# Kernel optimization log

Hardware: AMD Instinct MI355X
Metric: run time of the kernel (lower is better)

The kernel has to match this reference:

```python
import jax, jax.numpy as jnp
import numpy as np
from jax.scipy.special import logsumexp

B, T, D, H, K = 32, 512, 768, 256, 32


def setup_inputs() -> dict:
    key = jax.random.key(0)
    ks = jax.random.split(key, 12)
    x = jax.random.normal(ks[0], (B, T, D), jnp.float32)
    lengths = jax.random.randint(ks[1], (B,), T // 2, T + 1).astype(jnp.int32)
    mask = jnp.arange(T)[None, :] < lengths[:, None]  # [B,T] bool
    targets = jax.random.randint(ks[2], (B, T), 0, K)

    def p(k, shape, fan):
        return jax.random.normal(k, shape, jnp.float32) / np.sqrt(fan).astype(np.float32)

    W_ih_f = p(ks[3], (4 * H, D), D); W_hh_f = p(ks[4], (4 * H, H), H)
    W_ih_b = p(ks[5], (4 * H, D), D); W_hh_b = p(ks[6], (4 * H, H), H)
    b_f = jnp.zeros((4 * H,), jnp.float32); b_b = jnp.zeros((4 * H,), jnp.float32)
    W_clf = p(ks[7], (K, 2 * H), 2 * H); b_clf = jnp.zeros((K,), jnp.float32)
    start_t = jax.random.uniform(ks[8], (K,), jnp.float32, -0.1, 0.1)
    end_t = jax.random.uniform(ks[9], (K,), jnp.float32, -0.1, 0.1)
    trans = jax.random.uniform(ks[10], (K, K), jnp.float32, -0.1, 0.1)
    return {"input": x, "lengths": lengths, "mask": mask, "targets": targets,
            "W_ih_f": W_ih_f, "W_hh_f": W_hh_f, "b_f": b_f,
            "W_ih_b": W_ih_b, "W_hh_b": W_hh_b, "b_b": b_b,
            "W_clf": W_clf, "b_clf": b_clf,
            "start_t": start_t, "end_t": end_t, "trans": trans}


def _lstm_dir(x_tbd, W_ih, W_hh, b):
    # x_tbd: [T,B,D] -> hs [T,B,H], torch gate order (i,f,g,o)
    Hh = W_hh.shape[1]
    pre = jnp.einsum('tbd,gd->tbg', x_tbd, W_ih) + b  # precompute input projections

    def step(carry, p_t):
        h, c = carry
        g = p_t + h @ W_hh.T
        i, f, gg, o = jnp.split(g, 4, axis=-1)
        c = jax.nn.sigmoid(f) * c + jax.nn.sigmoid(i) * jnp.tanh(gg)
        h = jax.nn.sigmoid(o) * jnp.tanh(c)
        return (h, c), h

    b_sz = x_tbd.shape[1]
    init = (jnp.zeros((b_sz, Hh), x_tbd.dtype), jnp.zeros((b_sz, Hh), x_tbd.dtype))
    _, hs = jax.lax.scan(step, init, pre)
    return hs


def _emissions(x, lengths, W_ih_f, W_hh_f, b_f, W_ih_b, W_hh_b, b_b, W_clf, b_clf):
    Tn = x.shape[1]
    t_idx = jnp.arange(Tn)[None, :]
    # per-sequence reversal of the valid prefix (emulates packed bidirectional LSTM)
    rev_idx = jnp.where(t_idx < lengths[:, None], lengths[:, None] - 1 - t_idx, t_idx)
    h_f = _lstm_dir(x.transpose(1, 0, 2), W_ih_f, W_hh_f, b_f).transpose(1, 0, 2)
    x_rev = jnp.take_along_axis(x, rev_idx[:, :, None], axis=1)
    h_b = _lstm_dir(x_rev.transpose(1, 0, 2), W_ih_b, W_hh_b, b_b).transpose(1, 0, 2)
    h_b = jnp.take_along_axis(h_b, rev_idx[:, :, None], axis=1)  # un-flip
    hcat = jnp.concatenate([h_f, h_b], axis=-1)  # [B,T,2H]
    return hcat @ W_clf.T + b_clf  # [B,T,K]


def _crf_nll(em, targets, mask, lengths, start_t, end_t, trans):
    maskf = mask.astype(em.dtype)
    # numerator (gold path score)
    em_sc = jnp.take_along_axis(em, targets[:, :, None], axis=2)[..., 0]  # [B,T]
    tr_sc = trans[targets[:, :-1], targets[:, 1:]]  # [B,T-1]
    num = start_t[targets[:, 0]] + em_sc[:, 0] + jnp.sum((tr_sc + em_sc[:, 1:]) * maskf[:, 1:], axis=1)
    last_tags = jnp.take_along_axis(targets, (lengths - 1).astype(targets.dtype)[:, None], axis=1)[:, 0]
    num = num + end_t[last_tags]
    # log partition via forward algorithm
    def fwd_step(alpha, inp):
        e_t, m_t = inp
        nxt = logsumexp(alpha[:, :, None] + trans[None] + e_t[:, None, :], axis=1)
        return jnp.where(m_t[:, None], nxt, alpha), None

    alpha0 = start_t[None] + em[:, 0]
    alpha, _ = jax.lax.scan(fwd_step, alpha0, (em[:, 1:].transpose(1, 0, 2), mask[:, 1:].T))
    logZ = logsumexp(alpha + end_t[None], axis=1)
    return -jnp.mean(num - logZ)


def _viterbi(em, mask, start_t, end_t, trans):
    Kn = trans.shape[0]

    def vit_step(score, inp):
        e_t, m_t = inp
        bc = score[:, :, None] + trans[None] + e_t[:, None, :]  # [B,Kprev,Kcur]
        nxt = jnp.max(bc, axis=1)
        idx = jnp.argmax(bc, axis=1)  # [B,K] best previous tag
        idx = jnp.where(m_t[:, None], idx, jnp.arange(Kn)[None, :])  # identity on pads
        return jnp.where(m_t[:, None], nxt, score), idx

    score0 = start_t[None] + em[:, 0]
    score, hist = jax.lax.scan(vit_step, score0, (em[:, 1:].transpose(1, 0, 2), mask[:, 1:].T))
    last = jnp.argmax(score + end_t[None], axis=1)  # [B]

    def back(tag, h):
        prev = jnp.take_along_axis(h, tag[:, None], axis=1)[:, 0]
        return prev, prev

    _, tags_prev = jax.lax.scan(back, last, hist, reverse=True)  # [T-1,B]
    tags = jnp.concatenate([tags_prev, last[None]], axis=0).T  # [B,T]
    return jnp.where(mask, tags, 0)  # zero_pad


def reference(input, lengths, mask, targets, W_ih_f, W_hh_f, b_f, W_ih_b, W_hh_b, b_b,
              W_clf, b_clf, start_t, end_t, trans):
    em = _emissions(input, lengths, W_ih_f, W_hh_f, b_f, W_ih_b, W_hh_b, b_b, W_clf, b_clf)
    loss = _crf_nll(em, targets, mask, lengths, start_t, end_t, trans)
    preds = _viterbi(em, mask, start_t, end_t, trans)
    return loss, preds
```

## Files before the change

kernel.cpp:

```cpp
#include <hip/hip_runtime.h>
#include <hip/hip_bf16.h>


#define NB 32
#define NT 512
#define ND 768
#define NH 256
#define NK 32

__global__ __launch_bounds__(256) void k_sgemm(const float* __restrict__ A,
                                               const float* __restrict__ Wf,
                                               const float* __restrict__ Wb,
                                               float* __restrict__ C) {
    __shared__ float As[2][16][132];
    __shared__ float Bs[2][16][132];
    const int tid = threadIdx.x;
    const int bx = blockIdx.x;
    const int by = blockIdx.y;
    const int tx = tid & 15, ty = tid >> 4;
    const int sm = tid >> 2;
    const int sk = (tid & 3) * 4;
    float acc[8][8];
#pragma unroll
    for (int i = 0; i < 8; ++i)
#pragma unroll
        for (int j = 0; j < 8; ++j) acc[i][j] = 0.f;

    const float* Arow0 = A + (size_t)(by * 128 + sm) * ND + sk;
    const float* Arow1 = A + (size_t)(by * 128 + 64 + sm) * ND + sk;
    const int gn0 = bx * 128 + sm, gn1 = gn0 + 64;
    const float* W0 = (gn0 < 1024) ? (Wf + (size_t)gn0 * ND + sk) : (Wb + (size_t)(gn0 - 1024) * ND + sk);
    const float* W1 = (gn1 < 1024) ? (Wf + (size_t)gn1 * ND + sk) : (Wb + (size_t)(gn1 - 1024) * ND + sk);

    {
        float4 a0 = *(const float4*)(Arow0);
        float4 a1 = *(const float4*)(Arow1);
        float4 w0 = *(const float4*)(W0);
        float4 w1 = *(const float4*)(W1);
        As[0][sk + 0][sm] = a0.x; As[0][sk + 1][sm] = a0.y; As[0][sk + 2][sm] = a0.z; As[0][sk + 3][sm] = a0.w;
        As[0][sk + 0][64 + sm] = a1.x; As[0][sk + 1][64 + sm] = a1.y; As[0][sk + 2][64 + sm] = a1.z; As[0][sk + 3][64 + sm] = a1.w;
        Bs[0][sk + 0][sm] = w0.x; Bs[0][sk + 1][sm] = w0.y; Bs[0][sk + 2][sm] = w0.z; Bs[0][sk + 3][sm] = w0.w;
        Bs[0][sk + 0][64 + sm] = w1.x; Bs[0][sk + 1][64 + sm] = w1.y; Bs[0][sk + 2][64 + sm] = w1.z; Bs[0][sk + 3][64 + sm] = w1.w;
    }
    __syncthreads();

    int cur = 0;
    for (int k0 = 0; k0 < ND; k0 += 16) {
        const bool more = (k0 + 16) < ND;
        float4 na0, na1, nw0, nw1;
        if (more) {
            na0 = *(const float4*)(Arow0 + k0 + 16);
            na1 = *(const float4*)(Arow1 + k0 + 16);
            nw0 = *(const float4*)(W0 + k0 + 16);
            nw1 = *(const float4*)(W1 + k0 + 16);
        }
#pragma unroll
        for (int kk = 0; kk < 16; ++kk) {
            float a[8], b[8];
            *(float4*)&a[0] = *(const float4*)&As[cur][kk][ty * 4];
            *(float4*)&a[4] = *(const float4*)&As[cur][kk][64 + ty * 4];
            *(float4*)&b[0] = *(const float4*)&Bs[cur][kk][tx * 4];
            *(float4*)&b[4] = *(const float4*)&Bs[cur][kk][64 + tx * 4];
#pragma unroll
            for (int i = 0; i < 8; ++i)
#pragma unroll
                for (int j = 0; j < 8; ++j)
                    acc[i][j] = fmaf(a[i], b[j], acc[i][j]);
        }
        if (more) {
            const int nxt = cur ^ 1;
            As[nxt][sk + 0][sm] = na0.x; As[nxt][sk + 1][sm] = na0.y; As[nxt][sk + 2][sm] = na0.z; As[nxt][sk + 3][sm] = na0.w;
            As[nxt][sk + 0][64 + sm] = na1.x; As[nxt][sk + 1][64 + sm] = na1.y; As[nxt][sk + 2][64 + sm] = na1.z; As[nxt][sk + 3][64 + sm] = na1.w;
            Bs[nxt][sk + 0][sm] = nw0.x; Bs[nxt][sk + 1][sm] = nw0.y; Bs[nxt][sk + 2][sm] = nw0.z; Bs[nxt][sk + 3][sm] = nw0.w;
            Bs[nxt][sk + 0][64 + sm] = nw1.x; Bs[nxt][sk + 1][64 + sm] = nw1.y; Bs[nxt][sk + 2][64 + sm] = nw1.z; Bs[nxt][sk + 3][64 + sm] = nw1.w;
            __syncthreads();
            cur = nxt;
        }
    }
#pragma unroll
    for (int i = 0; i < 8; ++i) {
        int m = by * 128 + ((i < 4) ? (ty * 4 + i) : (64 + ty * 4 + (i - 4)));
        float* Crow = C + (size_t)m * 2048 + bx * 128;
        *(float4*)(Crow + tx * 4)      = make_float4(acc[i][0], acc[i][1], acc[i][2], acc[i][3]);
        *(float4*)(Crow + 64 + tx * 4) = make_float4(acc[i][4], acc[i][5], acc[i][6], acc[i][7]);
    }
}

__global__ __launch_bounds__(256) void k_wt4(const float* __restrict__ Whf,
                                             const float* __restrict__ Whb,
                                             float4* __restrict__ Wt4) {
    int gid = blockIdx.x * 256 + threadIdx.x;
    if (gid >= 131072) return;
    int dir = gid >> 16;
    int k   = (gid >> 8) & 255;
    int j   = gid & 255;
    const float* W = dir ? Whb : Whf;
    Wt4[gid] = make_float4(W[(size_t)(0 * 256 + j) * 256 + k],
                           W[(size_t)(1 * 256 + j) * 256 + k],
                           W[(size_t)(2 * 256 + j) * 256 + k],
                           W[(size_t)(3 * 256 + j) * 256 + k]);
}

__device__ __forceinline__ float sigm(float x) { return 1.f / (1.f + expf(-x)); }

__global__ __launch_bounds__(256, 1) void k_lstm6(const float* __restrict__ C,
                                                  const float4* __restrict__ Wt4,
                                                  const float* __restrict__ b_f,
                                                  const float* __restrict__ b_b,
                                                  const int* __restrict__ lengths,
                                                  float* __restrict__ h_f,
                                                  float* __restrict__ h_b) {
    __shared__ float4 wlds[36][256];
    __shared__ float hsh[4][272];
    const int tid = threadIdx.x;
    const int g = blockIdx.x & 63, s = blockIdx.x >> 6;
    const int b = g & 31, dir = g >> 5;
    const int j0 = s * 64;
    const float* bias = dir ? b_b : b_f;
    float* hdir = dir ? h_b : h_f;

    const int j = tid >> 2;
    const int kq = tid & 3;
    const int w = tid >> 6;
    const int lane = tid & 63;

    float4 wreg[28];
    {
        const float4* wb = Wt4 + ((size_t)dir * 256 + kq * 64) * 256 + j0 + j;
#pragma unroll
        for (int u = 0; u < 28; ++u) wreg[u] = wb[(size_t)u * 256];
#pragma unroll
        for (int u = 0; u < 36; ++u) wlds[u][tid] = wb[(size_t)(28 + u) * 256];
    }
    float4 breg = make_float4(0.f, 0.f, 0.f, 0.f);
    if (kq == 0)
        breg = make_float4(bias[j0 + j], bias[256 + j0 + j],
                           bias[512 + j0 + j], bias[768 + j0 + j]);
    const int mylen = lengths[b];
    float creg = 0.f;
    __syncthreads();

    for (int t = 0; t < NT; ++t) {
        float4 pre = make_float4(0.f, 0.f, 0.f, 0.f);
        if (kq == 0) {
            int src_t = t;
            if (dir) src_t = (t < mylen) ? (mylen - 1 - t) : t;
            const float* Crow = C + (size_t)(b * 512 + src_t) * 2048 + dir * 1024 + j0 + j;
            pre.x = Crow[0]; pre.y = Crow[256]; pre.z = Crow[512]; pre.w = Crow[768];
        }
        float4 acc = make_float4(0.f, 0.f, 0.f, 0.f);
        if (t > 0) {
            const float* hp = hdir + ((size_t)b * 512 + (t - 1)) * 256 + 4 * lane;
            unsigned long long u0, u1;
            int guard = 0;
            for (;;) {
                u0 = __hip_atomic_load((const unsigned long long*)hp,
                                       __ATOMIC_RELAXED, __HIP_MEMORY_SCOPE_AGENT);
                u1 = __hip_atomic_load((const unsigned long long*)(hp + 2),
                                       __ATOMIC_RELAXED, __HIP_MEMORY_SCOPE_AGENT);
                if ((unsigned)(u0 & 0xFFFFFFFFu) != 0xFFFFFFFFu &&
                    (unsigned)(u0 >> 32)        != 0xFFFFFFFFu &&
                    (unsigned)(u1 & 0xFFFFFFFFu) != 0xFFFFFFFFu &&
                    (unsigned)(u1 >> 32)        != 0xFFFFFFFFu) break;
                if (++guard > (1 << 22)) break;
            }
            const int d0 = 4 * lane;
            float* dst = &hsh[w][(d0 >> 6) * 68 + (d0 & 63)];
            *(float4*)dst = make_float4(
                __uint_as_float((unsigned)(u0 & 0xFFFFFFFFu)),
                __uint_as_float((unsigned)(u0 >> 32)),
                __uint_as_float((unsigned)(u1 & 0xFFFFFFFFu)),
                __uint_as_float((unsigned)(u1 >> 32)));
            asm volatile("s_waitcnt lgkmcnt(0)" ::: "memory");
            __builtin_amdgcn_sched_barrier(0);
            const float* src = &hsh[w][kq * 68];
#pragma unroll
            for (int c = 0; c < 16; ++c) {
                float ha[4];
                *(float4*)ha = *(const float4*)(src + 4 * c);
#pragma unroll
                for (int i = 0; i < 4; ++i) {
                    float4 wv = (c < 7) ? wreg[c * 4 + i] : wlds[(c - 7) * 4 + i][tid];
                    acc.x = fmaf(wv.x, ha[i], acc.x);
                    acc.y = fmaf(wv.y, ha[i], acc.y);
                    acc.z = fmaf(wv.z, ha[i], acc.z);
                    acc.w = fmaf(wv.w, ha[i], acc.w);
                }
            }
        }
        if (kq == 0) {
            acc.x += pre.x + breg.x; acc.y += pre.y + breg.y;
            acc.z += pre.z + breg.z; acc.w += pre.w + breg.w;
        }
#pragma unroll
        for (int off = 1; off <= 2; off <<= 1) {
            acc.x += __shfl_xor(acc.x, off);
            acc.y += __shfl_xor(acc.y, off);
            acc.z += __shfl_xor(acc.z, off);
            acc.w += __shfl_xor(acc.w, off);
        }
        float ig = sigm(acc.x), fg = sigm(acc.y), gt = tanhf(acc.z), og = sigm(acc.w);
        creg = fg * creg + ig * gt;
        float hn = og * tanhf(creg);
        if (kq == 0)
            __hip_atomic_store(hdir + ((size_t)b * 512 + t) * 256 + j0 + j, hn,
                               __ATOMIC_RELAXED, __HIP_MEMORY_SCOPE_AGENT);
    }
}

__global__ __launch_bounds__(256) void k_em(const float* __restrict__ hf,
                                            const float* __restrict__ hb,
                                            const float* __restrict__ Wclf,
                                            const float* __restrict__ bclf,
                                            const int* __restrict__ lengths,
                                            float* __restrict__ em) {
    extern __shared__ float4 wc4[];
    const int tid = threadIdx.x;
    for (int idx = tid; idx < 4096; idx += 256) {
        int jq = idx >> 5, ko = idx & 31;
        wc4[idx] = *(const float4*)(Wclf + (size_t)ko * 512 + jq * 4);
    }
    __syncthreads();
    const int r = tid >> 5, ko = tid & 31;
    const int m = blockIdx.x * 8 + r;
    const int b = m >> 9, t = m & 511;
    const int len = lengths[b];
    const int rev = (t < len) ? (len - 1 - t) : t;
    const float* hfr = hf + (size_t)m * 256;
    const float* hbr = hb + (size_t)(b * 512 + rev) * 256;
    float acc = bclf[ko];
#pragma unroll 4
    for (int jq = 0; jq < 64; ++jq) {
        float4 h4 = *(const float4*)(hfr + jq * 4);
        float4 ww = wc4[jq * 32 + ko];
        acc += h4.x * ww.x + h4.y * ww.y + h4.z * ww.z + h4.w * ww.w;
    }
#pragma unroll 4
    for (int jq = 0; jq < 64; ++jq) {
        float4 h4 = *(const float4*)(hbr + jq * 4);
        float4 ww = wc4[(64 + jq) * 32 + ko];
        acc += h4.x * ww.x + h4.y * ww.y + h4.z * ww.z + h4.w * ww.w;
    }
    em[(size_t)m * 32 + ko] = acc;
}

__global__ __launch_bounds__(64) void k_crfvit(const float* __restrict__ em,
                                               const int* __restrict__ targets,
                                               const int* __restrict__ lengths,
                                               const float* __restrict__ start_t,
                                               const float* __restrict__ end_t,
                                               const float* __restrict__ trans,
                                               float* __restrict__ numv,
                                               float* __restrict__ logZv,
                                               float* __restrict__ out) {
    __shared__ float trans_s[32][33];
    __shared__ float vec[32];
    __shared__ unsigned char hist[511 * 32];
    const int tid = threadIdx.x;
    const int b = blockIdx.x & 31;
    const int mode = blockIdx.x >> 5;
    for (int idx = tid; idx < 1024; idx += 64) trans_s[idx >> 5][idx & 31] = trans[idx];
    const int len = lengths[b];
    const float* emb = em + (size_t)b * 512 * 32;
    const int k = tid & 31, half = tid >> 5;
    if (tid < 32) vec[tid] = start_t[tid] + emb[tid];

    if (mode == 0) {
        float e_cur = emb[32 + k];
        for (int t = 1; t < NT; ++t) {
            float e_next = (t + 1 < NT) ? emb[(t + 1) * 32 + k] : 0.f;
            bool mv = t < len;
            int kp0 = half * 16;
            float m = -1e30f;
#pragma unroll 4
            for (int i = 0; i < 16; ++i)
                m = fmaxf(m, vec[kp0 + i] + trans_s[kp0 + i][k]);
            float m2 = fmaxf(m, __shfl_xor(m, 32));
            float ssum = 0.f;
#pragma unroll 4
            for (int i = 0; i < 16; ++i)
                ssum += __expf(vec[kp0 + i] + trans_s[kp0 + i][k] - m2);
            ssum += __shfl_xor(ssum, 32);
            float anew = m2 + __logf(ssum) + e_cur;
            if (half == 0 && mv) vec[k] = anew;
            e_cur = e_next;
        }
        float val = (tid < 32) ? vec[tid] + end_t[tid] : -1e30f;
        float m = val;
#pragma unroll
        for (int off = 32; off >= 1; off >>= 1) m = fmaxf(m, __shfl_xor(m, off));
        float e = (tid < 32) ? __expf(val - m) : 0.f;
#pragma unroll
        for (int off = 32; off >= 1; off >>= 1) e += __shfl_xor(e, off);
        if (tid == 0) logZv[b] = m + __logf(e);
        const int* tg = targets + b * 512;
        float partial = 0.f;
        for (int t = 1 + tid; t < NT; t += 64) {
            if (t < len) {
                int y0 = tg[t - 1], y1 = tg[t];
                partial += trans_s[y0][y1] + emb[t * 32 + y1];
            }
        }
#pragma unroll
        for (int off = 32; off >= 1; off >>= 1) partial += __shfl_xor(partial, off);
        if (tid == 0) {
            int y00 = tg[0];
            int yl = tg[len - 1];
            numv[b] = partial + start_t[y00] + emb[y00] + end_t[yl];
        }
    } else {
        float e_cur = emb[32 + k];
        for (int t = 1; t < NT; ++t) {
            float e_next = (t + 1 < NT) ? emb[(t + 1) * 32 + k] : 0.f;
            bool mv = t < len;
            int kp0 = half * 16;
            float e = e_cur;
            float m = -1e30f; int mi = kp0;
#pragma unroll 4
            for (int i = 0; i < 16; ++i) {
                float v = (vec[kp0 + i] + trans_s[kp0 + i][k]) + e;
                if (v > m) { m = v; mi = kp0 + i; }
            }
            float mo = __shfl_xor(m, 32);
            int io = __shfl_xor(mi, 32);
            float mlow = half ? mo : m;   int ilow = half ? io : mi;
            float mhigh = half ? m : mo;  int ihigh = half ? mi : io;
            float bm; int bi;
            if (mhigh > mlow) { bm = mhigh; bi = ihigh; } else { bm = mlow; bi = ilow; }
            if (half == 0) {
                hist[(t - 1) * 32 + k] = (unsigned char)(mv ? bi : k);
                if (mv) vec[k] = bm;
            }
            e_cur = e_next;
        }
        float val = (tid < 32) ? vec[tid] + end_t[tid] : -1e30f;
        int idx = (tid < 32) ? tid : 63;
#pragma unroll
        for (int off = 32; off >= 1; off >>= 1) {
            float vo = __shfl_xor(val, off);
            int io = __shfl_xor(idx, off);
            if (vo > val || (vo == val && io < idx)) { val = vo; idx = io; }
        }
        int cur = idx;
        float* ob = out + 1 + (size_t)b * 512;
        if (tid == 0) ob[511] = (511 < len) ? (float)cur : 0.f;
        for (int t2 = 510; t2 >= 0; --t2) {
            cur = hist[t2 * 32 + cur];
            if (tid == 0) ob[t2] = (t2 < len) ? (float)cur : 0.f;
        }
    }
}

__global__ __launch_bounds__(64) void k_loss(const float* __restrict__ numv,
                                             const float* __restrict__ logZv,
                                             float* __restrict__ out) {
    int tid = threadIdx.x;
    float v = (tid < 32) ? (logZv[tid] - numv[tid]) : 0.f;
#pragma unroll
    for (int off = 32; off >= 1; off >>= 1) v += __shfl_xor(v, off);
    if (tid == 0) out[0] = v / 32.f;
}

extern "C" void kernel_launch(void* const* d_in, const int* in_sizes, int n_in,
                              void* d_out, int out_size, void* d_ws, size_t ws_size,
                              hipStream_t stream) {
    const float* x       = (const float*)d_in[0];
    const int*   lengths = (const int*)d_in[1];
    const int*   targets = (const int*)d_in[3];
    const float* W_ih_f  = (const float*)d_in[4];
    const float* W_hh_f  = (const float*)d_in[5];
    const float* b_f     = (const float*)d_in[6];
    const float* W_ih_b  = (const float*)d_in[7];
    const float* W_hh_b  = (const float*)d_in[8];
    const float* b_b     = (const float*)d_in[9];
    const float* W_clf   = (const float*)d_in[10];
    const float* b_clf   = (const float*)d_in[11];
    const float* start_t = (const float*)d_in[12];
    const float* end_t   = (const float*)d_in[13];
    const float* trans   = (const float*)d_in[14];
    float* out = (float*)d_out;
    float* ws = (float*)d_ws;

    float* C     = ws;
    float* h_f   = C + (size_t)16384 * 2048;
    float* h_b   = h_f + (size_t)32 * 512 * 256;
    float* em    = h_b + (size_t)32 * 512 * 256;
    float4* Wt4  = (float4*)(em + (size_t)32 * 512 * 32);
    float* numv  = (float*)(Wt4 + 131072);
    float* logZv = numv + 32;

    hipMemsetAsync(h_f, 0xFF, (size_t)2 * 32 * 512 * 256 * sizeof(float), stream);
    k_wt4<<<512, 256, 0, stream>>>(W_hh_f, W_hh_b, Wt4);
    k_sgemm<<<dim3(16, 128), 256, 0, stream>>>(x, W_ih_f, W_ih_b, C);
    k_lstm6<<<256, 256, 0, stream>>>(C, Wt4, b_f, b_b, lengths, h_f, h_b);
    k_em<<<2048, 256, 65536, stream>>>(h_f, h_b, W_clf, b_clf, lengths, em);
    k_crfvit<<<64, 64, 0, stream>>>(em, targets, lengths, start_t, end_t, trans, numv, logZv, out);
    k_loss<<<1, 64, 0, stream>>>(numv, logZv, out);
}
```

Before: 2.437 ms.

## Use bf16 hi/lo split MFMA for input projection GEMM

Replaces the FP32 FMA-tiled GEMM for the LSTM input projections with MFMA 16x16x32 bf16 instructions. Each fp32 operand is split into high and low bf16 parts, and four MFMAs are accumulated to keep near-fp32 accuracy. Tiles are converted in registers and staged in LDS with a single buffer and two barriers per k-step. This trades extra MFMA work and conversion ALU for matrix-core throughput, and drops the previous double-buffered prefetch.

```diff
diff --git a/kernel.cpp b/kernel.cpp
--- a/kernel.cpp
+++ b/kernel.cpp
@@ -8,81 +8,99 @@
 #define NH 256
 #define NK 32
 
+using bf16x8 = __attribute__((ext_vector_type(8))) short;
+using f32x4  = __attribute__((ext_vector_type(4))) float;
+
+__device__ __forceinline__ ushort f2bf_rne(float f) {
+    unsigned u = __float_as_uint(f);
+    return (ushort)((u + 0x7FFFu + ((u >> 16) & 1u)) >> 16);
+}
+__device__ __forceinline__ float bf2f(ushort h) {
+    return __uint_as_float(((unsigned)h) << 16);
+}
+
 __global__ __launch_bounds__(256) void k_sgemm(const float* __restrict__ A,
                                                const float* __restrict__ Wf,
                                                const float* __restrict__ Wb,
                                                float* __restrict__ C) {
-    __shared__ float As[2][16][132];
-    __shared__ float Bs[2][16][132];
+    __shared__ ushort Ah[128][40], Al[128][40], Bh[128][40], Bl[128][40];
     const int tid = threadIdx.x;
     const int bx = blockIdx.x;
     const int by = blockIdx.y;
-    const int tx = tid & 15, ty = tid >> 4;
-    const int sm = tid >> 2;
-    const int sk = (tid & 3) * 4;
-    float acc[8][8];
-#pragma unroll
-    for (int i = 0; i < 8; ++i)
-#pragma unroll
-        for (int j = 0; j < 8; ++j) acc[i][j] = 0.f;
-
-    const float* Arow0 = A + (size_t)(by * 128 + sm) * ND + sk;
-    const float* Arow1 = A + (size_t)(by * 128 + 64 + sm) * ND + sk;
-    const int gn0 = bx * 128 + sm, gn1 = gn0 + 64;
-    const float* W0 = (gn0 < 1024) ? (Wf + (size_t)gn0 * ND + sk) : (Wb + (size_t)(gn0 - 1024) * ND + sk);
-    const float* W1 = (gn1 < 1024) ? (Wf + (size_t)gn1 * ND + sk) : (Wb + (size_t)(gn1 - 1024) * ND + sk);
-
-    {
-        float4 a0 = *(const float4*)(Arow0);
-        float4 a1 = *(const float4*)(Arow1);
-        float4 w0 = *(const float4*)(W0);
-        float4 w1 = *(const float4*)(W1);
-        As[0][sk + 0][sm] = a0.x; As[0][sk + 1][sm] = a0.y; As[0][sk + 2][sm] = a0.z; As[0][sk + 3][sm] = a0.w;
-        As[0][sk + 0][64 + sm] = a1.x; As[0][sk + 1][64 + sm] = a1.y; As[0][sk + 2][64 + sm] = a1.z; As[0][sk + 3][64 + sm] = a1.w;
-        Bs[0][sk + 0][sm] = w0.x; Bs[0][sk + 1][sm] = w0.y; Bs[0][sk + 2][sm] = w0.z; Bs[0][sk + 3][sm] = w0.w;
-        Bs[0][sk + 0][64 + sm] = w1.x; Bs[0][sk + 1][64 + sm] = w1.y; Bs[0][sk + 2][64 + sm] = w1.z; Bs[0][sk + 3][64 + sm] = w1.w;
-    }
-    __syncthreads();
-
-    int cur = 0;
-    for (int k0 = 0; k0 < ND; k0 += 16) {
-        const bool more = (k0 + 16) < ND;
-        float4 na0, na1, nw0, nw1;
-        if (more) {
-            na0 = *(const float4*)(Arow0 + k0 + 16);
-            na1 = *(const float4*)(Arow1 + k0 + 16);
-            nw0 = *(const float4*)(W0 + k0 + 16);
-            nw1 = *(const float4*)(W1 + k0 + 16);
-        }
-#pragma unroll
-        for (int kk = 0; kk < 16; ++kk) {
-            float a[8], b[8];
-            *(float4*)&a[0] = *(const float4*)&As[cur][kk][ty * 4];
-            *(float4*)&a[4] = *(const float4*)&As[cur][kk][64 + ty * 4];
-            *(float4*)&b[0] = *(const float4*)&Bs[cur][kk][tx * 4];
-            *(float4*)&b[4] = *(const float4*)&Bs[cur][kk][64 + tx * 4];
-#pragma unroll
-            for (int i = 0; i < 8; ++i)
-#pragma unroll
-                for (int j = 0; j < 8; ++j)
-                    acc[i][j] = fmaf(a[i], b[j], acc[i][j]);
-        }
-        if (more) {
-            const int nxt = cur ^ 1;
-            As[nxt][sk + 0][sm] = na0.x; As[nxt][sk + 1][sm] = na0.y; As[nxt][sk + 2][sm] = na0.z; As[nxt][sk + 3][sm] = na0.w;
-            As[nxt][sk + 0][64 + sm] = na1.x; As[nxt][sk + 1][64 + sm] = na1.y; As[nxt][sk + 2][64 + sm] = na1.z; As[nxt][sk + 3][64 + sm] = na1.w;
-            Bs[nxt][sk + 0][sm] = nw0.x; Bs[nxt][sk + 1][sm] = nw0.y; Bs[nxt][sk + 2][sm] = nw0.z; Bs[nxt][sk + 3][sm] = nw0.w;
-            Bs[nxt][sk + 0][64 + sm] = nw1.x; Bs[nxt][sk + 1][64 + sm] = nw1.y; Bs[nxt][sk + 2][64 + sm] = nw1.z; Bs[nxt][sk + 3][64 + sm] = nw1.w;
-            __syncthreads();
-            cur = nxt;
-        }
-    }
-#pragma unroll
-    for (int i = 0; i < 8; ++i) {
-        int m = by * 128 + ((i < 4) ? (ty * 4 + i) : (64 + ty * 4 + (i - 4)));
-        float* Crow = C + (size_t)m * 2048 + bx * 128;
-        *(float4*)(Crow + tx * 4)      = make_float4(acc[i][0], acc[i][1], acc[i][2], acc[i][3]);
-        *(float4*)(Crow + 64 + tx * 4) = make_float4(acc[i][4], acc[i][5], acc[i][6], acc[i][7]);
+    const int w = tid >> 6, lane = tid & 63;
+    const int l15 = lane & 15, koff = (lane >> 4) * 8;
+
+    const int srow = tid >> 1, shalf = tid & 1;
+    const float* Asrc = A + (size_t)(by * 128 + srow) * ND + shalf * 16;
+    const int gn = bx * 128 + srow;
+    const float* Bsrc = ((gn < 1024) ? (Wf + (size_t)gn * ND)
+                                     : (Wb + (size_t)(gn - 1024) * ND)) + shalf * 16;
+
+    f32x4 acc0[8], acc1[8];
+#pragma unroll
+    for (int ns = 0; ns < 8; ++ns) {
+        acc0[ns] = (f32x4){0.f, 0.f, 0.f, 0.f};
+        acc1[ns] = (f32x4){0.f, 0.f, 0.f, 0.f};
+    }
+
+    for (int k0 = 0; k0 < ND; k0 += 32) {
+        float fa[16], fb[16];
+        *(float4*)&fa[0]  = *(const float4*)(Asrc + k0 + 0);
+        *(float4*)&fa[4]  = *(const float4*)(Asrc + k0 + 4);
+        *(float4*)&fa[8]  = *(const float4*)(Asrc + k0 + 8);
+        *(float4*)&fa[12] = *(const float4*)(Asrc + k0 + 12);
+        *(float4*)&fb[0]  = *(const float4*)(Bsrc + k0 + 0);
+        *(float4*)&fb[4]  = *(const float4*)(Bsrc + k0 + 4);
+        *(float4*)&fb[8]  = *(const float4*)(Bsrc + k0 + 8);
+        *(float4*)&fb[12] = *(const float4*)(Bsrc + k0 + 12);
+        __syncthreads();
+        bf16x8 AH0, AH1, AL0, AL1, BH0, BH1, BL0, BL1;
+#pragma unroll
+        for (int i = 0; i < 8; ++i) {
+            ushort h;
+            h = f2bf_rne(fa[i]);     AH0[i] = (short)h; AL0[i] = (short)f2bf_rne(fa[i]     - bf2f(h));
+            h = f2bf_rne(fa[8 + i]); AH1[i] = (short)h; AL1[i] = (short)f2bf_rne(fa[8 + i] - bf2f(h));
+            h = f2bf_rne(fb[i]);     BH0[i] = (short)h; BL0[i] = (short)f2bf_rne(fb[i]     - bf2f(h));
+            h = f2bf_rne(fb[8 + i]); BH1[i] = (short)h; BL1[i] = (short)f2bf_rne(fb[8 + i] - bf2f(h));
+        }
+        {
+            const int c = shalf * 16;
+            *(bf16x8*)&Ah[srow][c] = AH0; *(bf16x8*)&Ah[srow][c + 8] = AH1;
+            *(bf16x8*)&Al[srow][c] = AL0; *(bf16x8*)&Al[srow][c + 8] = AL1;
+            *(bf16x8*)&Bh[srow][c] = BH0; *(bf16x8*)&Bh[srow][c + 8] = BH1;
+            *(bf16x8*)&Bl[srow][c] = BL0; *(bf16x8*)&Bl[srow][c + 8] = BL1;
+        }
+        __syncthreads();
+
+        bf16x8 a0h = *(const bf16x8*)&Ah[w * 32 + l15][koff];
+        bf16x8 a0l = *(const bf16x8*)&Al[w * 32 + l15][koff];
+        bf16x8 a1h = *(const bf16x8*)&Ah[w * 32 + 16 + l15][koff];
+        bf16x8 a1l = *(const bf16x8*)&Al[w * 32 + 16 + l15][koff];
+#pragma unroll
+        for (int ns = 0; ns < 8; ++ns) {
+            bf16x8 bh = *(const bf16x8*)&Bh[ns * 16 + l15][koff];
+            bf16x8 bl = *(const bf16x8*)&Bl[ns * 16 + l15][koff];
+            acc0[ns] = __builtin_amdgcn_mfma_f32_16x16x32_bf16(a0h, bh, acc0[ns], 0, 0, 0);
+            acc0[ns] = __builtin_amdgcn_mfma_f32_16x16x32_bf16(a0h, bl, acc0[ns], 0, 0, 0);
+            acc0[ns] = __builtin_amdgcn_mfma_f32_16x16x32_bf16(a0l, bh, acc0[ns], 0, 0, 0);
+            acc0[ns] = __builtin_amdgcn_mfma_f32_16x16x32_bf16(a0l, bl, acc0[ns], 0, 0, 0);
+            acc1[ns] = __builtin_amdgcn_mfma_f32_16x16x32_bf16(a1h, bh, acc1[ns], 0, 0, 0);
+            acc1[ns] = __builtin_amdgcn_mfma_f32_16x16x32_bf16(a1h, bl, acc1[ns], 0, 0, 0);
+            acc1[ns] = __builtin_amdgcn_mfma_f32_16x16x32_bf16(a1l, bh, acc1[ns], 0, 0, 0);
+            acc1[ns] = __builtin_amdgcn_mfma_f32_16x16x32_bf16(a1l, bl, acc1[ns], 0, 0, 0);
+        }
+    }
+    const int kg4 = (lane >> 4) * 4;
+#pragma unroll
+    for (int ns = 0; ns < 8; ++ns) {
+        const int gcol = bx * 128 + ns * 16 + l15;
+#pragma unroll
+        for (int r = 0; r < 4; ++r) {
+            int gm0 = by * 128 + w * 32 + kg4 + r;
+            C[(size_t)gm0 * 2048 + gcol] = acc0[ns][r];
+            int gm1 = gm0 + 16;
+            C[(size_t)gm1 * 2048 + gcol] = acc1[ns][r];
+        }
     }
 }
 
```

After: 2.081 ms. -14.6%, faster.
